# Performance work log

Measured on AMD Instinct MI355X. Metric: run time of the kernel, lower is better.

The kernel has to match this reference:

```python
import jax, jax.numpy as jnp
import numpy as np

B, N, S = 64, 128, 100          # batch, pod_num, seq_len
E, H, M = 64, 128, 3            # embed_dim, hidden_dim, modal_num
VOCAB = 2000
FIN = M * S * (E + 1)           # shared_encoder in_features = 19500
FG = M * H                      # gat feature dim = 384
MAX_EVENT_LEN = 100.0
LEAKY_ALPHA = 0.2


def setup_inputs() -> dict:
    key = jax.random.key(0)
    ks = jax.random.split(key, 16)
    inp = {
        "l_e": jax.random.randint(ks[0], (B, N, S), 0, VOCAB),
        "m_e": jax.random.randint(ks[1], (B, N, S), 0, VOCAB),
        "t_e": jax.random.randint(ks[2], (B, N, S), 0, VOCAB),
        "l_c": jax.random.uniform(ks[3], (B, N, S), jnp.float32) * 100.0,
        "m_c": jax.random.uniform(ks[4], (B, N, S), jnp.float32) * 100.0,
        "t_c": jax.random.uniform(ks[5], (B, N, S), jnp.float32) * 100.0,
        "adj": (jax.random.uniform(ks[6], (N, N)) > 0.5).astype(jnp.float32),
        # learned parameters (weights stored as (in, out); y = x @ W + b)
        "emb": jax.random.normal(ks[7], (VOCAB, E), jnp.float32) * 0.02,
        "W_se": jax.random.normal(ks[8], (FIN, 3 * H), jnp.float32) * (1.0 / np.sqrt(FIN)),
        "b_se": jnp.zeros((3 * H,), jnp.float32),
        "gat_W": jax.random.normal(ks[9], (FG, FG), jnp.float32) * (1.0 / np.sqrt(FG)),
        "gat_a": jax.random.normal(ks[10], (2 * FG, 1), jnp.float32) * 0.1,
        "W1": jax.random.normal(ks[11], (FG * N, N), jnp.float32) * (1.0 / np.sqrt(FG * N)),
        "b1": jnp.zeros((N,), jnp.float32),
    }
    return inp


def gat_layer(x, adj, W, a):
    """Faithful GraphAttentionLayer (concat=True, dropout=0) without materializing
    the [B,N,N,2F] a_input: e_ij = leakyrelu(a1.h_i + a2.h_j)."""
    h = x @ W                                      # [B,N,F]
    F_ = W.shape[1]
    a1, a2 = a[:F_, 0], a[F_:, 0]
    e = jax.nn.leaky_relu(
        (h @ a1)[:, :, None] + (h @ a2)[:, None, :], LEAKY_ALPHA
    )                                              # [B,N,N]
    att = jnp.where(adj > 0, e, -1e12)
    att = jax.nn.softmax(att, axis=-1)
    return jax.nn.relu(att @ h)                    # [B,N,F]


def reference(l_e, m_e, t_e, l_c, m_c, t_c, adj, emb, W_se, b_se, gat_W, gat_a, W1, b1):
    # embedding lookup + concat normalized event counts -> [B,N,S,E+1] per modality
    log_r = jnp.concatenate([emb[l_e], (l_c / MAX_EVENT_LEN)[..., None]], -1)
    metric_r = jnp.concatenate([emb[m_e], (m_c / MAX_EVENT_LEN)[..., None]], -1)
    trace_r = jnp.concatenate([emb[t_e], (t_c / MAX_EVENT_LEN)[..., None]], -1)
    # shared encoder: cat on feature dim, flatten per node, dense -> [B,N,3H]
    fused = jnp.concatenate([log_r, metric_r, trace_r], -1).reshape(B, N, -1)
    fusion_r = fused @ W_se + b_se
    # GAT + residual + linear head (use_gat_linear path)
    out = gat_layer(fusion_r, adj, gat_W, gat_a)
    x = fusion_r + out
    x = x.reshape(B, -1) @ W1 + b1                 # [B,N]
    return (x, fusion_r)
```

## Files before the change

kernel.cpp:

```cpp
#include <hip/hip_runtime.h>

#define KB_TOT 305
#define KPAD   19520
#define BROW   39040

typedef __attribute__((ext_vector_type(8))) short bf16x8_t;
typedef __attribute__((ext_vector_type(4))) float f32x4_t;

typedef const __attribute__((address_space(1))) unsigned int GAS_u32;
typedef __attribute__((address_space(3))) unsigned int LAS_u32;

__device__ inline unsigned short f2bf(float x) {
    union { float f; unsigned u; } a; a.f = x;
    unsigned r = a.u + 0x7fffu + ((a.u >> 16) & 1u);
    return (unsigned short)(r >> 16);
}
__device__ inline float bf2f(unsigned short h) {
    union { unsigned u; float f; } a; a.u = ((unsigned)h) << 16; return a.f;
}
__device__ inline unsigned long long pack4bf(float x, float y, float z, float w) {
    return (unsigned long long)f2bf(x) | ((unsigned long long)f2bf(y) << 16)
         | ((unsigned long long)f2bf(z) << 32) | ((unsigned long long)f2bf(w) << 48);
}

__global__ __launch_bounds__(256) void prep_kernel(
    const float* __restrict__ emb, const float* __restrict__ l_c,
    const float* __restrict__ m_c, const float* __restrict__ t_c,
    const float* __restrict__ W_se, const float* __restrict__ gat_W,
    unsigned short* __restrict__ ebf, unsigned short* __restrict__ Ac,
    unsigned short* __restrict__ WT, unsigned short* __restrict__ Bws) {
    __shared__ float tl[64 * 68];
    int bid = blockIdx.x, tid = threadIdx.x;
    if (bid < 125) {
        int i4 = (bid * 256 + tid) * 4;
        float4 v = *(const float4*)(emb + i4);
        *(unsigned long long*)(ebf + i4) = pack4bf(v.x, v.y, v.z, v.w);
    } else if (bid < 2685) {
        int lin = (bid - 125) * 256 + tid;
        int row = lin / 80, c4 = (lin - row * 80) * 4;
        float vv[4];
        #pragma unroll
        for (int ii = 0; ii < 4; ++ii) {
            int t = c4 + ii;
            float x = 0.f;
            if (t < 300) {
                int m = t / 100, s = t - m * 100;
                const float* C = (m == 0) ? l_c : ((m == 1) ? m_c : t_c);
                x = C[row * 100 + s] * 0.01f;
            }
            vv[ii] = x;
        }
        *(unsigned long long*)(Ac + row * 320 + c4) = pack4bf(vv[0], vv[1], vv[2], vv[3]);
    } else if (bid < 2721) {
        int idx = bid - 2685;
        int k0 = (idx % 6) * 64, n0 = (idx / 6) * 64;
        int rr = tid >> 2, c16 = (tid & 3) * 16;
        #pragma unroll
        for (int ii = 0; ii < 4; ++ii)
            *(float4*)(tl + rr * 68 + c16 + ii * 4) =
                *(const float4*)(gat_W + (k0 + rr) * 384 + n0 + c16 + ii * 4);
        __syncthreads();
        int c = tid >> 2, r16 = (tid & 3) * 16;
        unsigned long long* dst8 = (unsigned long long*)(WT + (n0 + c) * 384 + k0 + r16);
        #pragma unroll
        for (int q = 0; q < 4; ++q) {
            int rb = r16 + q * 4;
            dst8[q] = pack4bf(tl[(rb + 0) * 68 + c], tl[(rb + 1) * 68 + c],
                              tl[(rb + 2) * 68 + c], tl[(rb + 3) * 68 + c]);
        }
    } else {
        int idx = bid - 2721;
        int kb = idx % 305, h0 = (idx / 305) * 64;
        int rr = tid >> 2, c16 = (tid & 3) * 16;
        float4 v[4];
        if (kb < 300) {
            int m = kb / 100, s = kb - m * 100;
            const float* srcp = W_se + (s * 195 + m * 65 + rr) * 384 + h0 + c16;
            #pragma unroll
            for (int ii = 0; ii < 4; ++ii) v[ii] = *(const float4*)(srcp + ii * 4);
        } else {
            int t = (kb - 300) * 64 + rr;
            if (t < 300) {
                int m = t / 100, s = t - m * 100;
                const float* srcp = W_se + (s * 195 + m * 65 + 64) * 384 + h0 + c16;
                #pragma unroll
                for (int ii = 0; ii < 4; ++ii) v[ii] = *(const float4*)(srcp + ii * 4);
            } else {
                #pragma unroll
                for (int ii = 0; ii < 4; ++ii) v[ii] = make_float4(0.f, 0.f, 0.f, 0.f);
            }
        }
        #pragma unroll
        for (int ii = 0; ii < 4; ++ii) *(float4*)(tl + rr * 68 + c16 + ii * 4) = v[ii];
        __syncthreads();
        int c = tid >> 2, r16 = (tid & 3) * 16;
        unsigned long long* dst8 =
            (unsigned long long*)(Bws + (unsigned)(h0 + c) * KPAD + kb * 64 + r16);
        #pragma unroll
        for (int q = 0; q < 4; ++q) {
            int rb = r16 + q * 4;
            dst8[q] = pack4bf(tl[(rb + 0) * 68 + c], tl[(rb + 1) * 68 + c],
                              tl[(rb + 2) * 68 + c], tl[(rb + 3) * 68 + c]);
        }
    }
}

__global__ __launch_bounds__(256) void gemm_fused_kernel(
    const int* __restrict__ l_e, const int* __restrict__ m_e, const int* __restrict__ t_e,
    const unsigned short* __restrict__ emb_bf, const unsigned short* __restrict__ Ac_bf,
    const unsigned short* __restrict__ Bws, float* __restrict__ fusion_d,
    unsigned short* __restrict__ Pbf) {

    __shared__ alignas(16) unsigned short Al[128 * 64];
    __shared__ alignas(16) unsigned short Bl[128 * 64];

    const int tid  = threadIdx.x;
    const int lane = tid & 63;
    const int wid  = tid >> 6;

    int bid = blockIdx.x;
    int lin = (bid & 7) * 144 + (bid >> 3);
    const int mt = lin % 64;
    int rest = lin / 64;
    const int nt = rest % 3;
    const int kc = rest / 3;
    const int bm0 = mt * 128;
    const int h0  = nt * 128;
    int kb        = kc * 51;
    const int kbe = (kb + 51 < KB_TOT) ? kb + 51 : KB_TOT;

    const int l7 = lane & 7, l3 = lane >> 3;
    const int voffA = ((l7 ^ l3) << 4);
    const int rowg0 = bm0 + wid * 32 + l3;

    f32x4_t acc[4][4];
    #pragma unroll
    for (int i = 0; i < 4; ++i)
        #pragma unroll
        for (int j = 0; j < 4; ++j) acc[i][j] = (f32x4_t){0.f, 0.f, 0.f, 0.f};

    const int wr = wid >> 1, wc = wid & 1;
    const int l15 = lane & 15, l4 = lane >> 4;

    int idx4[4];
    if (kb < 300) {
        int m = kb / 100, s = kb - m * 100;
        const int* I = (m == 0) ? l_e : ((m == 1) ? m_e : t_e);
        const int* Ib = I + rowg0 * 100 + s;
        idx4[0] = Ib[0]; idx4[1] = Ib[800]; idx4[2] = Ib[1600]; idx4[3] = Ib[2400];
    }

    for (; kb < kbe; ++kb) {
        if (kb < 300) {
            #pragma unroll
            for (int p = 0; p < 4; ++p) {
                const char* src = (const char*)emb_bf + ((long)idx4[p] << 7) + voffA;
                __builtin_amdgcn_global_load_lds((GAS_u32*)src,
                    (LAS_u32*)((char*)Al + (wid * 4 + p) * 1024), 16, 0, 0);
            }
        } else {
            int q = kb - 300;
            #pragma unroll
            for (int p = 0; p < 4; ++p) {
                const char* src = (const char*)Ac_bf + (long)(rowg0 + p * 8) * 640
                                + q * 128 + voffA;
                __builtin_amdgcn_global_load_lds((GAS_u32*)src,
                    (LAS_u32*)((char*)Al + (wid * 4 + p) * 1024), 16, 0, 0);
            }
        }
        #pragma unroll
        for (int p = 0; p < 4; ++p) {
            int ch = wid * 4 + p;
            int hl = ch * 8 + l3;
            long gb = (long)(h0 + hl) * BROW + kb * 128 + ((l7 << 4) ^ (l3 << 4));
            __builtin_amdgcn_global_load_lds((GAS_u32*)((const char*)Bws + gb),
                                             (LAS_u32*)((char*)Bl + ch * 1024), 16, 0, 0);
        }
        int kn = kb + 1;
        if (kn < 300 && kn < kbe) {
            int m = kn / 100, s = kn - m * 100;
            const int* I = (m == 0) ? l_e : ((m == 1) ? m_e : t_e);
            const int* Ib = I + rowg0 * 100 + s;
            idx4[0] = Ib[0]; idx4[1] = Ib[800]; idx4[2] = Ib[1600]; idx4[3] = Ib[2400];
        }
        __syncthreads();
        #pragma unroll
        for (int ks = 0; ks < 2; ++ks) {
            int kb2 = ks * 64 + l4 * 16;
            bf16x8_t af[4], bfr[4];
            #pragma unroll
            for (int i = 0; i < 4; ++i) {
                int row = wr * 64 + i * 16 + l15;
                af[i]  = *(const bf16x8_t*)((const char*)Al + row * 128 + (kb2 ^ ((row & 7) << 4)));
                int col = wc * 64 + i * 16 + l15;
                bfr[i] = *(const bf16x8_t*)((const char*)Bl + col * 128 + (kb2 ^ ((col & 7) << 4)));
            }
            #pragma unroll
            for (int i = 0; i < 4; ++i)
                #pragma unroll
                for (int j = 0; j < 4; ++j)
                    acc[i][j] = __builtin_amdgcn_mfma_f32_16x16x32_bf16(af[i], bfr[j], acc[i][j], 0, 0, 0);
        }
        __syncthreads();
    }
    if (kc == 0) {
        #pragma unroll
        for (int i = 0; i < 4; ++i)
            #pragma unroll
            for (int j = 0; j < 4; ++j)
                #pragma unroll
                for (int r = 0; r < 4; ++r) {
                    int row = bm0 + wr * 64 + i * 16 + l4 * 4 + r;
                    int col = h0 + wc * 64 + j * 16 + l15;
                    fusion_d[row * 384 + col] = acc[i][j][r];
                }
    } else {
        unsigned short* dst = Pbf + (size_t)(kc - 1) * 3145728;
        #pragma unroll
        for (int i = 0; i < 4; ++i)
            #pragma unroll
            for (int j = 0; j < 4; ++j)
                #pragma unroll
                for (int r = 0; r < 4; ++r) {
                    int row = bm0 + wr * 64 + i * 16 + l4 * 4 + r;
                    int col = h0 + wc * 64 + j * 16 + l15;
                    dst[row * 384 + col] = f2bf(acc[i][j][r]);
                }
    }
}

__global__ __launch_bounds__(256) void reduce_fusion_kernel(float* __restrict__ fusion_d,
                                                            const unsigned short* __restrict__ Pbf,
                                                            const float* __restrict__ b_se,
                                                            unsigned short* __restrict__ fusion_bf,
                                                            float* __restrict__ e_ws) {
    if (blockIdx.x < 16) {
        int z = blockIdx.x * 1024 + threadIdx.x * 4;
        *(float4*)(e_ws + z) = make_float4(0.f, 0.f, 0.f, 0.f);
    }
    int i4 = blockIdx.x * 256 + threadIdx.x;
    int col4 = (i4 % 96) * 4;
    float4 a = *(const float4*)(fusion_d + i4 * 4);
    float4 bs = *(const float4*)(b_se + col4);
    float s0 = a.x + bs.x, s1 = a.y + bs.y, s2 = a.z + bs.z, s3 = a.w + bs.w;
    #pragma unroll
    for (int sl = 0; sl < 5; ++sl) {
        ushort4 p = *(const ushort4*)(Pbf + (size_t)sl * 3145728 + i4 * 4);
        s0 += bf2f(p.x); s1 += bf2f(p.y); s2 += bf2f(p.z); s3 += bf2f(p.w);
    }
    *(float4*)(fusion_d + i4 * 4) = make_float4(s0, s1, s2, s3);
    *(unsigned long long*)(fusion_bf + i4 * 4) = pack4bf(s0, s1, s2, s3);
}

__global__ __launch_bounds__(256) void gat_h_kernel(const unsigned short* __restrict__ fusion_bf,
                                                    const unsigned short* __restrict__ WT,
                                                    const float* __restrict__ gat_a,
                                                    unsigned short* __restrict__ hT,
                                                    float* __restrict__ e_ws) {
    __shared__ alignas(16) unsigned short Al[128 * 64];
    __shared__ alignas(16) unsigned short Bl[128 * 64];
    const int tid  = threadIdx.x;
    const int lane = tid & 63;
    const int wid  = tid >> 6;
    const int b  = blockIdx.x;
    const int c0 = blockIdx.y * 128;
    const int l7 = lane & 7, l3 = lane >> 3;
    const int voffA = ((l7 ^ l3) << 4);
    const int wr = wid >> 1, wc = wid & 1;
    const int l15 = lane & 15, l4 = lane >> 4;

    f32x4_t acc[4][4];
    #pragma unroll
    for (int i = 0; i < 4; ++i)
        #pragma unroll
        for (int j = 0; j < 4; ++j) acc[i][j] = (f32x4_t){0.f, 0.f, 0.f, 0.f};

    for (int kb = 0; kb < 6; ++kb) {
        #pragma unroll
        for (int p = 0; p < 4; ++p) {
            int ch = wid * 4 + p;
            int rl = ch * 8 + l3;
            long ga = (long)(b * 128 + rl) * 768 + kb * 128 + voffA;
            __builtin_amdgcn_global_load_lds((GAS_u32*)((const char*)fusion_bf + ga),
                                             (LAS_u32*)((char*)Al + ch * 1024), 16, 0, 0);
            long gb = (long)(c0 + rl) * 768 + kb * 128 + voffA;
            __builtin_amdgcn_global_load_lds((GAS_u32*)((const char*)WT + gb),
                                             (LAS_u32*)((char*)Bl + ch * 1024), 16, 0, 0);
        }
        __syncthreads();
        #pragma unroll
        for (int ks = 0; ks < 2; ++ks) {
            int kb2 = ks * 64 + l4 * 16;
            bf16x8_t af[4], bfr[4];
            #pragma unroll
            for (int i = 0; i < 4; ++i) {
                int row = wr * 64 + i * 16 + l15;
                af[i]  = *(const bf16x8_t*)((const char*)Al + row * 128 + (kb2 ^ ((row & 7) << 4)));
                int col = wc * 64 + i * 16 + l15;
                bfr[i] = *(const bf16x8_t*)((const char*)Bl + col * 128 + (kb2 ^ ((col & 7) << 4)));
            }
            #pragma unroll
            for (int i = 0; i < 4; ++i)
                #pragma unroll
                for (int j = 0; j < 4; ++j)
                    acc[i][j] = __builtin_amdgcn_mfma_f32_16x16x32_bf16(af[i], bfr[j], acc[i][j], 0, 0, 0);
        }
        __syncthreads();
    }
    #pragma unroll
    for (int i = 0; i < 4; ++i)
        #pragma unroll
        for (int j = 0; j < 4; ++j) {
            int nb = wr * 64 + i * 16 + l4 * 4;
            int f  = c0 + wc * 64 + j * 16 + l15;
            *(unsigned long long*)(hT + ((size_t)(b * 384 + f)) * 128 + nb) =
                pack4bf(acc[i][j][0], acc[i][j][1], acc[i][j][2], acc[i][j][3]);
        }
    float a1v[4], a2v[4];
    #pragma unroll
    for (int j = 0; j < 4; ++j) {
        int f = c0 + wc * 64 + j * 16 + l15;
        a1v[j] = gat_a[f];
        a2v[j] = gat_a[384 + f];
    }
    #pragma unroll
    for (int i = 0; i < 4; ++i)
        #pragma unroll
        for (int r = 0; r < 4; ++r) {
            float p1 = 0.f, p2 = 0.f;
            #pragma unroll
            for (int j = 0; j < 4; ++j) {
                float hv = acc[i][j][r];
                p1 += hv * a1v[j];
                p2 += hv * a2v[j];
            }
            #pragma unroll
            for (int m = 1; m < 16; m <<= 1) {
                p1 += __shfl_xor(p1, m);
                p2 += __shfl_xor(p2, m);
            }
            if (l15 == 0) {
                int n = wr * 64 + i * 16 + l4 * 4 + r;
                atomicAdd(&e_ws[b * 128 + n], p1);
                atomicAdd(&e_ws[8192 + b * 128 + n], p2);
            }
        }
}

__global__ __launch_bounds__(256) void gat_pv_kernel(const float* __restrict__ e_ws,
                                                     const float* __restrict__ adj,
                                                     const unsigned short* __restrict__ hT,
                                                     const float* __restrict__ fusion_d,
                                                     unsigned short* __restrict__ x_pre_bf) {
    __shared__ alignas(16) unsigned short Pl[128 * 128];
    __shared__ alignas(16) unsigned short Bl[128 * 128];
    __shared__ float se2[128];
    const int tid  = threadIdx.x;
    const int lane = tid & 63;
    const int wid  = tid >> 6;
    const int b  = blockIdx.x;
    const int f0 = blockIdx.y * 128;
    const int wr = wid >> 1, wc = wid & 1;
    const int l15 = lane & 15, l4 = lane >> 4;

    if (tid < 128) se2[tid] = e_ws[8192 + b * 128 + tid];
    #pragma unroll
    for (int p = 0; p < 8; ++p) {
        int ch = wid * 8 + p;
        int row = ch * 4 + (lane >> 4);
        long gb = (long)(b * 384 + f0 + row) * 256 + (((lane & 15) ^ (row & 7)) << 4);
        __builtin_amdgcn_global_load_lds((GAS_u32*)((const char*)hT + gb),
                                         (LAS_u32*)((char*)Bl + ch * 1024), 16, 0, 0);
    }
    __syncthreads();

    {
        int r = tid >> 1, half = tid & 1;
        float er = e_ws[b * 128 + r];
        const float* arow = adj + r * 128 + half * 64;
        const float* e2h = se2 + half * 64;
        float mx = -1e30f;
        #pragma unroll 8
        for (int j = 0; j < 64; ++j) {
            float v = er + e2h[j];
            v = (v > 0.f) ? v : 0.2f * v;
            v = (arow[j] > 0.f) ? v : -1e12f;
            mx = fmaxf(mx, v);
        }
        mx = fmaxf(mx, __shfl_xor(mx, 1));
        float sum = 0.f;
        #pragma unroll 8
        for (int j = 0; j < 64; ++j) {
            float v = er + e2h[j];
            v = (v > 0.f) ? v : 0.2f * v;
            v = (arow[j] > 0.f) ? v : -1e12f;
            sum += __expf(v - mx);
        }
        sum += __shfl_xor(sum, 1);
        float inv = 1.f / sum;
        #pragma unroll
        for (int g = 0; g < 8; ++g) {
            float vv[8];
            #pragma unroll
            for (int q = 0; q < 8; ++q) {
                int j = g * 8 + q;
                float v = er + e2h[j];
                v = (v > 0.f) ? v : 0.2f * v;
                v = (arow[j] > 0.f) ? v : -1e12f;
                vv[q] = __expf(v - mx) * inv;
            }
            char* dst = (char*)Pl + r * 256 + ((half * 128 + g * 16) ^ ((r & 7) << 4));
            *(unsigned long long*)dst       = pack4bf(vv[0], vv[1], vv[2], vv[3]);
            *(unsigned long long*)(dst + 8) = pack4bf(vv[4], vv[5], vv[6], vv[7]);
        }
    }
    __syncthreads();

    f32x4_t acc[4][4];
    #pragma unroll
    for (int i = 0; i < 4; ++i)
        #pragma unroll
        for (int j = 0; j < 4; ++j) acc[i][j] = (f32x4_t){0.f, 0.f, 0.f, 0.f};

    #pragma unroll
    for (int st = 0; st < 4; ++st) {
        int ko = st * 64 + l4 * 16;
        bf16x8_t af[4], bfr[4];
        #pragma unroll
        for (int i = 0; i < 4; ++i) {
            int row = wr * 64 + i * 16 + l15;
            af[i]  = *(const bf16x8_t*)((const char*)Pl + row * 256 + (ko ^ ((row & 7) << 4)));
            int col = wc * 64 + i * 16 + l15;
            bfr[i] = *(const bf16x8_t*)((const char*)Bl + col * 256 + (ko ^ ((col & 7) << 4)));
        }
        #pragma unroll
        for (int i = 0; i < 4; ++i)
            #pragma unroll
            for (int j = 0; j < 4; ++j)
                acc[i][j] = __builtin_amdgcn_mfma_f32_16x16x32_bf16(af[i], bfr[j], acc[i][j], 0, 0, 0);
    }
    #pragma unroll
    for (int i = 0; i < 4; ++i)
        #pragma unroll
        for (int j = 0; j < 4; ++j) {
            int f = f0 + wc * 64 + j * 16 + l15;
            #pragma unroll
            for (int r = 0; r < 4; ++r) {
                int n = wr * 64 + i * 16 + l4 * 4 + r;
                float v = acc[i][j][r];
                v = (v > 0.f ? v : 0.f) + fusion_d[(b * 128 + n) * 384 + f];
                x_pre_bf[(size_t)b * 49152 + n * 384 + f] = f2bf(v);
            }
        }
}

__global__ __launch_bounds__(256) void final_kernel(const unsigned short* __restrict__ x_pre_bf,
                                                    const float* __restrict__ W1,
                                                    float* __restrict__ pf) {
    int n = blockIdx.x;
    int q = blockIdx.y;
    __shared__ float xl[64 * 196];
    int tid = threadIdx.x;
    #pragma unroll
    for (int p = 0; p < 6; ++p) {
        int e = p * 2048 + tid * 8;
        int b = e / 192, f = e - b * 192;
        bf16x8_t v8 = *(const bf16x8_t*)(x_pre_bf + (size_t)b * 49152 + n * 384 + q * 192 + f);
        float* d = xl + b * 196 + f;
        #pragma unroll
        for (int ii = 0; ii < 8; ++ii) d[ii] = bf2f((unsigned short)v8[ii]);
    }
    __syncthreads();
    int col = (tid & 31) * 4, bh = tid >> 5;
    float acc[8][4] = {};
    #pragma unroll 2
    for (int f = 0; f < 192; ++f) {
        float4 w = *(const float4*)(W1 + ((size_t)(n * 384 + q * 192 + f)) * 128 + col);
        #pragma unroll
        for (int bb = 0; bb < 8; ++bb) {
            float xv = xl[(bh * 8 + bb) * 196 + f];
            acc[bb][0] += xv * w.x; acc[bb][1] += xv * w.y;
            acc[bb][2] += xv * w.z; acc[bb][3] += xv * w.w;
        }
    }
    int slot = n * 2 + q;
    #pragma unroll
    for (int bb = 0; bb < 8; ++bb) {
        int b = bh * 8 + bb;
        *(float4*)(pf + (size_t)slot * 8192 + b * 128 + col) =
            make_float4(acc[bb][0], acc[bb][1], acc[bb][2], acc[bb][3]);
    }
}

__global__ __launch_bounds__(256) void reduce_final_kernel(const float* __restrict__ pf,
                                                           const float* __restrict__ b1,
                                                           float* __restrict__ xout) {
    int i = blockIdx.x * 256 + threadIdx.x;
    float acc = 0.f;
    for (int s = 0; s < 256; ++s) acc += pf[(size_t)s * 8192 + i];
    xout[i] = acc + b1[i & 127];
}

extern "C" void kernel_launch(void* const* d_in, const int* in_sizes, int n_in,
                              void* d_out, int out_size, void* d_ws, size_t ws_size,
                              hipStream_t stream) {
    (void)in_sizes; (void)n_in; (void)out_size; (void)ws_size;
    const int*   l_e   = (const int*)d_in[0];
    const int*   m_e   = (const int*)d_in[1];
    const int*   t_e   = (const int*)d_in[2];
    const float* l_c   = (const float*)d_in[3];
    const float* m_c   = (const float*)d_in[4];
    const float* t_c   = (const float*)d_in[5];
    const float* adj   = (const float*)d_in[6];
    const float* emb   = (const float*)d_in[7];
    const float* W_se  = (const float*)d_in[8];
    const float* b_se  = (const float*)d_in[9];
    const float* gat_W = (const float*)d_in[10];
    const float* gat_a = (const float*)d_in[11];
    const float* W1    = (const float*)d_in[12];
    const float* b1    = (const float*)d_in[13];

    float* xout     = (float*)d_out;
    float* fusion_d = xout + 8192;

    char* ws = (char*)d_ws;
    unsigned short* Bws    = (unsigned short*)(ws);
    unsigned short* emb_bf = (unsigned short*)(ws + 15728640);
    unsigned short* Ac_bf  = (unsigned short*)(ws + 15990784);
    unsigned short* WT_bf  = (unsigned short*)(ws + 21233664);
    unsigned short* Pbf    = (unsigned short*)(ws + 21528576);
    unsigned short* fusion_bf = (unsigned short*)(ws);
    unsigned short* hT_bf     = (unsigned short*)(ws + 6291456);
    unsigned short* x_pre_bf  = (unsigned short*)(ws + 12582912);
    float*          e_ws      = (float*)(ws + 18874368);
    float*          pf        = (float*)(ws + 21528576);

    prep_kernel<<<4551, 256, 0, stream>>>(emb, l_c, m_c, t_c, W_se, gat_W,
                                          emb_bf, Ac_bf, WT_bf, Bws);
    gemm_fused_kernel<<<1152, 256, 0, stream>>>(l_e, m_e, t_e, emb_bf, Ac_bf, Bws, fusion_d, Pbf);
    reduce_fusion_kernel<<<3072, 256, 0, stream>>>(fusion_d, Pbf, b_se, fusion_bf, e_ws);
    gat_h_kernel<<<dim3(64, 3), 256, 0, stream>>>(fusion_bf, WT_bf, gat_a, hT_bf, e_ws);
    gat_pv_kernel<<<dim3(64, 3), 256, 0, stream>>>(e_ws, adj, hT_bf, fusion_d, x_pre_bf);
    final_kernel<<<dim3(128, 2), 256, 0, stream>>>(x_pre_bf, W1, pf);
    reduce_final_kernel<<<32, 256, 0, stream>>>(pf, b1, xout);
}
```

Measured before the change: 373.0 us.

## Move final linear head to bf16 MFMA and reduce split-K slices

```diff
diff --git a/kernel.cpp b/kernel.cpp
--- a/kernel.cpp
+++ b/kernel.cpp
@@ -27,8 +27,10 @@
     const float* __restrict__ emb, const float* __restrict__ l_c,
     const float* __restrict__ m_c, const float* __restrict__ t_c,
     const float* __restrict__ W_se, const float* __restrict__ gat_W,
+    const float* __restrict__ W1,
     unsigned short* __restrict__ ebf, unsigned short* __restrict__ Ac,
-    unsigned short* __restrict__ WT, unsigned short* __restrict__ Bws) {
+    unsigned short* __restrict__ WT, unsigned short* __restrict__ Bws,
+    unsigned short* __restrict__ W1T) {
     __shared__ float tl[64 * 68];
     int bid = blockIdx.x, tid = threadIdx.x;
     if (bid < 125) {
@@ -68,7 +70,7 @@
             dst8[q] = pack4bf(tl[(rb + 0) * 68 + c], tl[(rb + 1) * 68 + c],
                               tl[(rb + 2) * 68 + c], tl[(rb + 3) * 68 + c]);
         }
-    } else {
+    } else if (bid < 4551) {
         int idx = bid - 2721;
         int kb = idx % 305, h0 = (idx / 305) * 64;
         int rr = tid >> 2, c16 = (tid & 3) * 16;
@@ -102,6 +104,24 @@
             dst8[q] = pack4bf(tl[(rb + 0) * 68 + c], tl[(rb + 1) * 68 + c],
                               tl[(rb + 2) * 68 + c], tl[(rb + 3) * 68 + c]);
         }
+    } else {
+        int idx = bid - 4551;
+        int k0 = (idx % 768) * 64, n0 = (idx / 768) * 64;
+        int rr = tid >> 2, c16 = (tid & 3) * 16;
+        #pragma unroll
+        for (int ii = 0; ii < 4; ++ii)
+            *(float4*)(tl + rr * 68 + c16 + ii * 4) =
+                *(const float4*)(W1 + (size_t)(k0 + rr) * 128 + n0 + c16 + ii * 4);
+        __syncthreads();
+        int c = tid >> 2, r16 = (tid & 3) * 16;
+        unsigned long long* dst8 =
+            (unsigned long long*)(W1T + (size_t)(n0 + c) * 49152 + k0 + r16);
+        #pragma unroll
+        for (int q = 0; q < 4; ++q) {
+            int rb = r16 + q * 4;
+            dst8[q] = pack4bf(tl[(rb + 0) * 68 + c], tl[(rb + 1) * 68 + c],
+                              tl[(rb + 2) * 68 + c], tl[(rb + 3) * 68 + c]);
+        }
     }
 }
 
@@ -119,15 +139,15 @@
     const int wid  = tid >> 6;
 
     int bid = blockIdx.x;
-    int lin = (bid & 7) * 144 + (bid >> 3);
+    int lin = (bid & 7) * 96 + (bid >> 3);
     const int mt = lin % 64;
     int rest = lin / 64;
     const int nt = rest % 3;
     const int kc = rest / 3;
     const int bm0 = mt * 128;
     const int h0  = nt * 128;
-    int kb        = kc * 51;
-    const int kbe = (kb + 51 < KB_TOT) ? kb + 51 : KB_TOT;
+    int kb        = (kc == 0) ? 0 : (77 + (kc - 1) * 76);
+    const int kbe = 77 + kc * 76 > KB_TOT ? KB_TOT : 77 + kc * 76;
 
     const int l7 = lane & 7, l3 = lane >> 3;
     const int voffA = ((l7 ^ l3) << 4);
@@ -244,7 +264,7 @@
     float4 bs = *(const float4*)(b_se + col4);
     float s0 = a.x + bs.x, s1 = a.y + bs.y, s2 = a.z + bs.z, s3 = a.w + bs.w;
     #pragma unroll
-    for (int sl = 0; sl < 5; ++sl) {
+    for (int sl = 0; sl < 3; ++sl) {
         ushort4 p = *(const ushort4*)(Pbf + (size_t)sl * 3145728 + i4 * 4);
         s0 += bf2f(p.x); s1 += bf2f(p.y); s2 += bf2f(p.z); s3 += bf2f(p.w);
     }
@@ -455,41 +475,77 @@
 }
 
 __global__ __launch_bounds__(256) void final_kernel(const unsigned short* __restrict__ x_pre_bf,
-                                                    const float* __restrict__ W1,
+                                                    const unsigned short* __restrict__ W1T,
                                                     float* __restrict__ pf) {
-    int n = blockIdx.x;
-    int q = blockIdx.y;
-    __shared__ float xl[64 * 196];
-    int tid = threadIdx.x;
-    #pragma unroll
-    for (int p = 0; p < 6; ++p) {
-        int e = p * 2048 + tid * 8;
-        int b = e / 192, f = e - b * 192;
-        bf16x8_t v8 = *(const bf16x8_t*)(x_pre_bf + (size_t)b * 49152 + n * 384 + q * 192 + f);
-        float* d = xl + b * 196 + f;
-        #pragma unroll
-        for (int ii = 0; ii < 8; ++ii) d[ii] = bf2f((unsigned short)v8[ii]);
-    }
-    __syncthreads();
-    int col = (tid & 31) * 4, bh = tid >> 5;
-    float acc[8][4] = {};
-    #pragma unroll 2
-    for (int f = 0; f < 192; ++f) {
-        float4 w = *(const float4*)(W1 + ((size_t)(n * 384 + q * 192 + f)) * 128 + col);
-        #pragma unroll
-        for (int bb = 0; bb < 8; ++bb) {
-            float xv = xl[(bh * 8 + bb) * 196 + f];
-            acc[bb][0] += xv * w.x; acc[bb][1] += xv * w.y;
-            acc[bb][2] += xv * w.z; acc[bb][3] += xv * w.w;
-        }
-    }
-    int slot = n * 2 + q;
-    #pragma unroll
-    for (int bb = 0; bb < 8; ++bb) {
-        int b = bh * 8 + bb;
-        *(float4*)(pf + (size_t)slot * 8192 + b * 128 + col) =
-            make_float4(acc[bb][0], acc[bb][1], acc[bb][2], acc[bb][3]);
-    }
+    __shared__ alignas(16) unsigned short Al[64 * 64];
+    __shared__ alignas(16) unsigned short Bl[128 * 64];
+    const int tid  = threadIdx.x;
+    const int lane = tid & 63;
+    const int wid  = tid >> 6;
+    const int kc   = blockIdx.x;
+    const int l7 = lane & 7, l3 = lane >> 3;
+    const int voffA = ((l7 ^ l3) << 4);
+    const int l15 = lane & 15, l4 = lane >> 4;
+
+    f32x4_t acc[4][2];
+    #pragma unroll
+    for (int i = 0; i < 4; ++i) {
+        acc[i][0] = (f32x4_t){0.f, 0.f, 0.f, 0.f};
+        acc[i][1] = (f32x4_t){0.f, 0.f, 0.f, 0.f};
+    }
+
+    for (int ks = 0; ks < 3; ++ks) {
+        #pragma unroll
+        for (int p = 0; p < 2; ++p) {
+            int ch = wid * 2 + p;
+            int row = ch * 8 + l3;
+            long ga = (long)row * 98304 + kc * 384 + ks * 128 + voffA;
+            __builtin_amdgcn_global_load_lds((GAS_u32*)((const char*)x_pre_bf + ga),
+                                             (LAS_u32*)((char*)Al + ch * 1024), 16, 0, 0);
+        }
+        #pragma unroll
+        for (int p = 0; p < 4; ++p) {
+            int ch = wid * 4 + p;
+            int col = ch * 8 + l3;
+            long gb = (long)col * 98304 + kc * 384 + ks * 128 + voffA;
+            __builtin_amdgcn_global_load_lds((GAS_u32*)((const char*)W1T + gb),
+                                             (LAS_u32*)((char*)Bl + ch * 1024), 16, 0, 0);
+        }
+        __syncthreads();
+        #pragma unroll
+        for (int ks2 = 0; ks2 < 2; ++ks2) {
+            int kb2 = ks2 * 64 + l4 * 16;
+            bf16x8_t af[4], bfr[2];
+            #pragma unroll
+            for (int i = 0; i < 4; ++i) {
+                int row = i * 16 + l15;
+                af[i] = *(const bf16x8_t*)((const char*)Al + row * 128 + (kb2 ^ ((row & 7) << 4)));
+            }
+            #pragma unroll
+            for (int j = 0; j < 2; ++j) {
+                int col = wid * 32 + j * 16 + l15;
+                bfr[j] = *(const bf16x8_t*)((const char*)Bl + col * 128 + (kb2 ^ ((col & 7) << 4)));
+            }
+            #pragma unroll
+            for (int i = 0; i < 4; ++i) {
+                acc[i][0] = __builtin_amdgcn_mfma_f32_16x16x32_bf16(af[i], bfr[0], acc[i][0], 0, 0, 0);
+                acc[i][1] = __builtin_amdgcn_mfma_f32_16x16x32_bf16(af[i], bfr[1], acc[i][1], 0, 0, 0);
+            }
+        }
+        __syncthreads();
+    }
+    float* dst = pf + (size_t)kc * 8192;
+    #pragma unroll
+    for (int i = 0; i < 4; ++i)
+        #pragma unroll
+        for (int j = 0; j < 2; ++j) {
+            int col = wid * 32 + j * 16 + l15;
+            #pragma unroll
+            for (int r = 0; r < 4; ++r) {
+                int row = i * 16 + l4 * 4 + r;
+                dst[row * 128 + col] = acc[i][j][r];
+            }
+        }
 }
 
 __global__ __launch_bounds__(256) void reduce_final_kernel(const float* __restrict__ pf,
@@ -497,6 +553,7 @@
                                                            float* __restrict__ xout) {
     int i = blockIdx.x * 256 + threadIdx.x;
     float acc = 0.f;
+    #pragma unroll 8
     for (int s = 0; s < 256; ++s) acc += pf[(size_t)s * 8192 + i];
     xout[i] = acc + b1[i & 127];
 }
@@ -529,18 +586,19 @@
     unsigned short* Ac_bf  = (unsigned short*)(ws + 15990784);
     unsigned short* WT_bf  = (unsigned short*)(ws + 21233664);
     unsigned short* Pbf    = (unsigned short*)(ws + 21528576);
+    unsigned short* W1T_bf = (unsigned short*)(ws + 40402944);
     unsigned short* fusion_bf = (unsigned short*)(ws);
     unsigned short* hT_bf     = (unsigned short*)(ws + 6291456);
     unsigned short* x_pre_bf  = (unsigned short*)(ws + 12582912);
     float*          e_ws      = (float*)(ws + 18874368);
     float*          pf        = (float*)(ws + 21528576);
 
-    prep_kernel<<<4551, 256, 0, stream>>>(emb, l_c, m_c, t_c, W_se, gat_W,
-                                          emb_bf, Ac_bf, WT_bf, Bws);
-    gemm_fused_kernel<<<1152, 256, 0, stream>>>(l_e, m_e, t_e, emb_bf, Ac_bf, Bws, fusion_d, Pbf);
+    prep_kernel<<<6087, 256, 0, stream>>>(emb, l_c, m_c, t_c, W_se, gat_W, W1,
+                                          emb_bf, Ac_bf, WT_bf, Bws, W1T_bf);
+    gemm_fused_kernel<<<768, 256, 0, stream>>>(l_e, m_e, t_e, emb_bf, Ac_bf, Bws, fusion_d, Pbf);
     reduce_fusion_kernel<<<3072, 256, 0, stream>>>(fusion_d, Pbf, b_se, fusion_bf, e_ws);
     gat_h_kernel<<<dim3(64, 3), 256, 0, stream>>>(fusion_bf, WT_bf, gat_a, hT_bf, e_ws);
     gat_pv_kernel<<<dim3(64, 3), 256, 0, stream>>>(e_ws, adj, hT_bf, fusion_d, x_pre_bf);
-    final_kernel<<<dim3(128, 2), 256, 0, stream>>>(x_pre_bf, W1, pf);
+    final_kernel<<<256, 256, 0, stream>>>(x_pre_bf, W1T_bf, pf);
     reduce_final_kernel<<<32, 256, 0, stream>>>(pf, b1, xout);
 }
```

Result: faster. 319.9 us (-14.2%).
